# Performance work log

Measured on AMD Instinct MI355X. Metric: run time of the kernel, lower is better.

The kernel has to match this reference:

```python
import jax, jax.numpy as jnp
import numpy as np

N_NODES = 50000
N_EDGES = 500000
F_IN = 16      # node feature dim F
F_OUT = 16     # channels F_
E_FEAT = 8     # edge feature dim
HIDDEN = 32    # kernel_network hidden size


def _glorot(key, shape):
    fan_in, fan_out = shape[0], shape[1]
    lim = np.sqrt(6.0 / (fan_in + fan_out)).astype(np.float32)
    return jax.random.uniform(key, shape, jnp.float32, -lim, lim)


def setup_inputs() -> dict:
    key = jax.random.key(0)
    ks = jax.random.split(key, 8)
    x = jax.random.normal(ks[0], (N_NODES, F_IN), jnp.float32)
    e = jax.random.uniform(ks[1], (N_EDGES, E_FEAT), jnp.float32)
    idx_i = jax.random.randint(ks[2], (N_EDGES,), 0, N_NODES, jnp.int32)  # targets
    idx_j = jax.random.randint(ks[3], (N_EDGES,), 0, N_NODES, jnp.int32)  # sources
    W1 = _glorot(ks[4], (E_FEAT, HIDDEN))
    b1 = jnp.zeros((HIDDEN,), jnp.float32)
    W2 = _glorot(ks[5], (HIDDEN, F_OUT * F_IN))
    b2 = jnp.zeros((F_OUT * F_IN,), jnp.float32)
    root_kernel = _glorot(ks[6], (F_IN, F_OUT))
    bias = jnp.zeros((F_OUT,), jnp.float32)
    return {"x": x, "e": e, "idx_i": idx_i, "idx_j": idx_j,
            "W1": W1, "b1": b1, "W2": W2, "b2": b2,
            "root_kernel": root_kernel, "bias": bias}


def reference(x, e, idx_i, idx_j, W1, b1, W2, b2, root_kernel, bias):
    # Edge-conditioned filter-generating network (MLP, relu hidden, linear out)
    h = jax.nn.relu(e @ W1 + b1)                       # [E, HIDDEN]
    kern = (h @ W2 + b2).reshape(-1, F_IN, F_OUT)      # [E, F, F_]
    # gather source node features, per-edge matmul, scatter-add to targets
    msg = jnp.einsum('ef,efc->ec', x[idx_j], kern)     # [E, F_]
    out = jax.ops.segment_sum(msg, idx_i, num_segments=N_NODES)  # [N, F_]
    out = out + x @ root_kernel + bias
    return out
```

## Files before the change

kernel.cpp:

```cpp
#include <hip/hip_runtime.h>

typedef __attribute__((ext_vector_type(8))) _Float16 f16x8_t;
typedef __attribute__((ext_vector_type(2))) _Float16 f16x2_t;
typedef __attribute__((ext_vector_type(4))) float f32x4_t;

__device__ __forceinline__ f16x2_t pkh(float lo, float hi) {
    return __builtin_bit_cast(f16x2_t, __builtin_amdgcn_cvt_pkrtz(lo, hi));
}
__device__ __forceinline__ unsigned int pkrtz(float lo, float hi) {
    return __builtin_bit_cast(unsigned int, __builtin_amdgcn_cvt_pkrtz(lo, hi));
}

#define LD4(p) (*reinterpret_cast<const float4*>(p))


__global__ __launch_bounds__(256) void prep_kernel(
    const float* __restrict__ x,
    const float* __restrict__ W1,
    const float* __restrict__ b1,
    const float* __restrict__ W2,
    const float* __restrict__ b2,
    const float* __restrict__ rootk,
    const float* __restrict__ bias,
    float* __restrict__ out,
    _Float16* __restrict__ tab,
    int n_nodes, int root_blocks)
{
    const int tid = threadIdx.x;
    const int bid = blockIdx.x;

    if (bid < root_blocks) {
        __shared__ float sR[256];
        __shared__ float sB[16];
        if (tid < 256) sR[tid] = rootk[tid];
        if (tid < 16)  sB[tid] = bias[tid];
        __syncthreads();

        int nid = bid * 256 + tid;
        if (nid >= n_nodes) return;

        const float* xp = x + (size_t)nid * 16;
        float xf[16];
#pragma unroll
        for (int f = 0; f < 16; f += 4) {
            float4 v = LD4(xp + f);
            xf[f] = v.x; xf[f + 1] = v.y; xf[f + 2] = v.z; xf[f + 3] = v.w;
        }
        float o[16];
#pragma unroll
        for (int cc = 0; cc < 16; ++cc) o[cc] = sB[cc];
#pragma unroll
        for (int f = 0; f < 16; ++f) {
            float p = xf[f];
#pragma unroll
            for (int cc = 0; cc < 16; ++cc)
                o[cc] = fmaf(p, sR[f * 16 + cc], o[cc]);
        }
        float* dst = out + (size_t)nid * 16;
#pragma unroll
        for (int cc = 0; cc < 16; cc += 4)
            *reinterpret_cast<float4*>(dst + cc) = make_float4(o[cc], o[cc+1], o[cc+2], o[cc+3]);
    } else {
        for (int it = tid; it < 64 * 19; it += 256) {
            int grp  = it >> 6;
            int lane = it & 63;
            int q = lane >> 4, cc = lane & 15;
            union { _Float16 h[8]; uint4 u; } pk;
            if (grp < 2) {
                int hh = grp;
#pragma unroll
                for (int j = 0; j < 8; ++j) {
                    float v = 0.f;
                    if (q == 0)              v = W1[j * 32 + cc + 16 * hh];
                    else if (q == 1 && j==0) v = b1[cc + 16 * hh];
                    pk.h[j] = (_Float16)v;
                }
                *reinterpret_cast<uint4*>(tab + ((size_t)hh * 64 + lane) * 8) = pk.u;
            } else {
                int s = grp - 2;
#pragma unroll
                for (int j = 0; j < 8; ++j) {
                    float v;
                    if (s < 16) {
                        int hd = (j < 4) ? (4 * q + j) : (4 * q + 12 + j);
                        v = W2[hd * 256 + s * 16 + cc];
                    } else {
                        v = (q < 2) ? b2[(q * 8 + j) * 16 + cc] : 0.f;
                    }
                    pk.h[j] = (_Float16)v;
                }
                *reinterpret_cast<uint4*>(tab + 1024 + ((size_t)s * 64 + lane) * 8) = pk.u;
            }
        }
    }
}

__device__ __forceinline__ float4 shfl4(float4 v, int src) {
    float4 r;
    r.x = __shfl(v.x, src); r.y = __shfl(v.y, src);
    r.z = __shfl(v.z, src); r.w = __shfl(v.w, src);
    return r;
}

template<int EXACT>
__global__ __launch_bounds__(256) void edge_mfma_kernel(
    const float* __restrict__ x,
    const float* __restrict__ efeat,
    const int*   __restrict__ idx_i,
    const int*   __restrict__ idx_j,
    const _Float16* __restrict__ tab,
    float* __restrict__ out,
    int n_edges, int n_groups)
{
    const int lane = threadIdx.x & 63;
    const int q = lane >> 4;
    const int c = lane & 15;

    const f16x8_t* w1f = reinterpret_cast<const f16x8_t*>(tab) + lane;
    const f16x8_t aW1_0 = w1f[0];
    const f16x8_t aW1_1 = w1f[64];
    const f16x8_t* w2f = reinterpret_cast<const f16x8_t*>(tab + 1024) + lane;
    f16x8_t bW2[17];
#pragma unroll
    for (int s = 0; s < 17; ++s) bW2[s] = w2f[s * 64];

    const unsigned int c1 = (q == 1) ? 0x00003C00u : 0u;
    const bool isq0 = (q == 0);
    const bool qodd = (q & 1);
    float* const outc = out + c;

    const int wid = blockIdx.x * 4 + (threadIdx.x >> 6);
    const int g0  = wid * 4;
    if (g0 >= n_groups) return;
    const int rem = n_groups - g0;

    auto ldj = [&](int gg) -> int {
        int eid = gg * 16 + c;
        if (!EXACT) { if (eid >= n_edges) eid = n_edges - 1; }
        return idx_j[eid];
    };
    auto eptr = [&](int gg) -> const float* {
        int eid = gg * 16 + c;
        if (!EXACT) { if (eid >= n_edges) eid = n_edges - 1; }
        return efeat + (size_t)eid * 8;
    };

    auto compute = [&](float4 XQ, float4 E0, float4 E1, int gg) {
        int t0, t1, t2, t3;
        if (EXACT || (gg * 16 + 16 <= n_edges)) {
            int4 tv = *reinterpret_cast<const int4*>(idx_i + gg * 16 + q * 4);
            t0 = tv.x; t1 = tv.y; t2 = tv.z; t3 = tv.w;
        } else {
            const int eb = gg * 16 + q * 4;
            t0 = (eb + 0 < n_edges) ? idx_i[eb + 0] : 0;
            t1 = (eb + 1 < n_edges) ? idx_i[eb + 1] : 0;
            t2 = (eb + 2 < n_edges) ? idx_i[eb + 2] : 0;
            t3 = (eb + 3 < n_edges) ? idx_i[eb + 3] : 0;
        }

        float4 X0 = shfl4(XQ, c);
        float4 X1 = shfl4(XQ, c + 16);
        float4 X2 = shfl4(XQ, c + 32);
        float4 X3 = shfl4(XQ, c + 48);

        union { f16x8_t v8; f16x2_t v2[4]; unsigned int u[4]; } bB;
        bB.u[0] = isq0 ? pkrtz(E0.x, E0.y) : c1;
        bB.u[1] = isq0 ? pkrtz(E0.z, E0.w) : 0u;
        bB.u[2] = isq0 ? pkrtz(E1.x, E1.y) : 0u;
        bB.u[3] = isq0 ? pkrtz(E1.z, E1.w) : 0u;

        f32x4_t z4 = {0.f, 0.f, 0.f, 0.f};
        f32x4_t h0 = __builtin_amdgcn_mfma_f32_16x16x32_f16(aW1_0, bB.v8, z4, 0, 0, 0);
        f32x4_t h1 = __builtin_amdgcn_mfma_f32_16x16x32_f16(aW1_1, bB.v8, z4, 0, 0, 0);

        f16x2_t hp0 = pkh(fmaxf(h0[0], 0.f), fmaxf(h0[1], 0.f));
        f16x2_t hp1 = pkh(fmaxf(h0[2], 0.f), fmaxf(h0[3], 0.f));
        f16x2_t hp2 = pkh(fmaxf(h1[0], 0.f), fmaxf(h1[1], 0.f));
        f16x2_t hp3 = pkh(fmaxf(h1[2], 0.f), fmaxf(h1[3], 0.f));

        float xf[16];
        xf[0]=X0.x; xf[1]=X0.y; xf[2]=X0.z; xf[3]=X0.w;
        xf[4]=X1.x; xf[5]=X1.y; xf[6]=X1.z; xf[7]=X1.w;
        xf[8]=X2.x; xf[9]=X2.y; xf[10]=X2.z; xf[11]=X2.w;
        xf[12]=X3.x; xf[13]=X3.y; xf[14]=X3.z; xf[15]=X3.w;

        f16x2_t xss[16];
#pragma unroll
        for (int f = 0; f < 16; ++f)
            xss[f] = pkh(xf[f], xf[f]);

        union { f16x8_t v8; unsigned int u[4]; } xb;
        xb.u[0] = pkrtz(qodd ? xf[8]  : xf[0], qodd ? xf[9]  : xf[1]);
        xb.u[1] = pkrtz(qodd ? xf[10] : xf[2], qodd ? xf[11] : xf[3]);
        xb.u[2] = pkrtz(qodd ? xf[12] : xf[4], qodd ? xf[13] : xf[5]);
        xb.u[3] = pkrtz(qodd ? xf[14] : xf[6], qodd ? xf[15] : xf[7]);

        f32x4_t acc0 = {0.f, 0.f, 0.f, 0.f};
        f32x4_t acc1 = {0.f, 0.f, 0.f, 0.f};
        union { f16x8_t v8; f16x2_t v2[4]; } afr;
#pragma unroll
        for (int s = 0; s < 16; s += 2) {
            f16x2_t xs2 = xss[s];
            afr.v2[0] = hp0 * xs2;
            afr.v2[1] = hp1 * xs2;
            afr.v2[2] = hp2 * xs2;
            afr.v2[3] = hp3 * xs2;
            acc0 = __builtin_amdgcn_mfma_f32_16x16x32_f16(afr.v8, bW2[s], acc0, 0, 0, 0);
            xs2 = xss[s + 1];
            afr.v2[0] = hp0 * xs2;
            afr.v2[1] = hp1 * xs2;
            afr.v2[2] = hp2 * xs2;
            afr.v2[3] = hp3 * xs2;
            acc1 = __builtin_amdgcn_mfma_f32_16x16x32_f16(afr.v8, bW2[s + 1], acc1, 0, 0, 0);
        }
        acc0 = __builtin_amdgcn_mfma_f32_16x16x32_f16(xb.v8, bW2[16], acc0, 0, 0, 0);

        const float rr0 = acc0[0] + acc1[0];
        const float rr1 = acc0[1] + acc1[1];
        const float rr2 = acc0[2] + acc1[2];
        const float rr3 = acc0[3] + acc1[3];
        if (EXACT) {
            atomicAdd(outc + (size_t)t0 * 16, rr0);
            atomicAdd(outc + (size_t)t1 * 16, rr1);
            atomicAdd(outc + (size_t)t2 * 16, rr2);
            atomicAdd(outc + (size_t)t3 * 16, rr3);
        } else {
            const int eb = gg * 16 + q * 4;
            if (eb + 0 < n_edges) atomicAdd(outc + (size_t)t0 * 16, rr0);
            if (eb + 1 < n_edges) atomicAdd(outc + (size_t)t1 * 16, rr1);
            if (eb + 2 < n_edges) atomicAdd(outc + (size_t)t2 * 16, rr2);
            if (eb + 3 < n_edges) atomicAdd(outc + (size_t)t3 * 16, rr3);
        }
    };

#define STAGE(BXQ, BE0, BE1, jv, gg)                                \
    {                                                               \
        BXQ = LD4(x + (size_t)(jv) * 16 + q * 4);                   \
        const float* ep = eptr(gg);                                 \
        BE0 = LD4(ep); BE1 = LD4(ep + 4);                           \
    }

    const int jA = ldj(g0);
    const int jB = (rem > 1) ? ldj(g0 + 1) : 0;
    const int jC = (rem > 2) ? ldj(g0 + 2) : 0;
    const int jD = (rem > 3) ? ldj(g0 + 3) : 0;

    float4 aq, ae0, ae1;
    float4 bq, be0, be1;

    STAGE(aq, ae0, ae1, jA, g0);
    if (rem > 1) STAGE(bq, be0, be1, jB, g0 + 1);
    compute(aq, ae0, ae1, g0);
    if (rem > 1) {
        if (rem > 2) STAGE(aq, ae0, ae1, jC, g0 + 2);
        compute(bq, be0, be1, g0 + 1);
        if (rem > 2) {
            if (rem > 3) STAGE(bq, be0, be1, jD, g0 + 3);
            compute(aq, ae0, ae1, g0 + 2);
            if (rem > 3) compute(bq, be0, be1, g0 + 3);
        }
    }
#undef STAGE
}

extern "C" void kernel_launch(void* const* d_in, const int* in_sizes, int n_in,
                              void* d_out, int out_size, void* d_ws, size_t ws_size,
                              hipStream_t stream) {
    const float* x     = (const float*)d_in[0];
    const float* e     = (const float*)d_in[1];
    const int*   idx_i = (const int*)d_in[2];
    const int*   idx_j = (const int*)d_in[3];
    const float* W1    = (const float*)d_in[4];
    const float* b1    = (const float*)d_in[5];
    const float* W2    = (const float*)d_in[6];
    const float* b2    = (const float*)d_in[7];
    const float* rootk = (const float*)d_in[8];
    const float* bias  = (const float*)d_in[9];

    int n_nodes  = in_sizes[0] / 16;
    int n_edges  = in_sizes[2];
    int n_groups = (n_edges + 15) / 16;

    float* out = (float*)d_out;
    _Float16* tab = (_Float16*)d_ws;

    int root_blocks = (n_nodes + 255) / 256;
    prep_kernel<<<root_blocks + 1, 256, 0, stream>>>(x, W1, b1, W2, b2, rootk, bias,
                                                     out, tab, n_nodes, root_blocks);

    int blocks = (n_groups + 15) / 16;
    if ((n_edges & 15) == 0)
        edge_mfma_kernel<1><<<blocks, 256, 0, stream>>>(x, e, idx_i, idx_j, tab, out,
                                                        n_edges, n_groups);
    else
        edge_mfma_kernel<0><<<blocks, 256, 0, stream>>>(x, e, idx_i, idx_j, tab, out,
                                                        n_edges, n_groups);
}
```

Measured before the change: 46.22 us.

## Bucket edges by target node to reduce scatter atomics

Adds a bucketing pass that atomically counts each edge's target and stores edge ids in fixed per-node slots, with an overflow list handled by a scalar fallback kernel. A node-centric MFMA kernel then processes each node's incoming edges, reduces the messages in registers, and issues one atomic per output channel per node instead of one per edge. The old edge kernel is kept as a fallback when the workspace is too small and is changed to a grid-stride form. The cost is an extra pass with 500k atomics, a scattered write of edge ids, and poor wave utilisation: average degree is about 10, so each wave runs one 16-edge chunk per node with many lanes idle, and edge features are now gathered randomly.

```diff
diff --git a/kernel.cpp b/kernel.cpp
--- a/kernel.cpp
+++ b/kernel.cpp
@@ -4,6 +4,9 @@
 typedef __attribute__((ext_vector_type(2))) _Float16 f16x2_t;
 typedef __attribute__((ext_vector_type(4))) float f32x4_t;
 
+#define SLOTS 64
+#define OVF_CAP 8192
+
 __device__ __forceinline__ f16x2_t pkh(float lo, float hi) {
     return __builtin_bit_cast(f16x2_t, __builtin_amdgcn_cvt_pkrtz(lo, hi));
 }
@@ -12,6 +15,13 @@
 }
 
 #define LD4(p) (*reinterpret_cast<const float4*>(p))
+
+__device__ __forceinline__ float4 shfl4(float4 v, int src) {
+    float4 r;
+    r.x = __shfl(v.x, src); r.y = __shfl(v.y, src);
+    r.z = __shfl(v.z, src); r.w = __shfl(v.w, src);
+    return r;
+}
 
 
 __global__ __launch_bounds__(256) void prep_kernel(
@@ -24,6 +34,8 @@
     const float* __restrict__ bias,
     float* __restrict__ out,
     _Float16* __restrict__ tab,
+    int* __restrict__ cnt,
+    int* __restrict__ ovf_cnt,
     int n_nodes, int root_blocks)
 {
     const int tid = threadIdx.x;
@@ -38,6 +50,7 @@
 
         int nid = bid * 256 + tid;
         if (nid >= n_nodes) return;
+        if (cnt) cnt[nid] = 0;
 
         const float* xp = x + (size_t)nid * 16;
         float xf[16];
@@ -61,6 +74,7 @@
         for (int cc = 0; cc < 16; cc += 4)
             *reinterpret_cast<float4*>(dst + cc) = make_float4(o[cc], o[cc+1], o[cc+2], o[cc+3]);
     } else {
+        if (tid == 0 && ovf_cnt) *ovf_cnt = 0;
         for (int it = tid; it < 64 * 19; it += 256) {
             int grp  = it >> 6;
             int lane = it & 63;
@@ -95,27 +109,190 @@
     }
 }
 
-__device__ __forceinline__ float4 shfl4(float4 v, int src) {
-    float4 r;
-    r.x = __shfl(v.x, src); r.y = __shfl(v.y, src);
-    r.z = __shfl(v.z, src); r.w = __shfl(v.w, src);
-    return r;
-}
-
-template<int EXACT>
-__global__ __launch_bounds__(256) void edge_mfma_kernel(
+__global__ __launch_bounds__(256) void bucket_kernel(
+    const int* __restrict__ idx_i,
+    int* __restrict__ cnt,
+    int* __restrict__ eord,
+    int* __restrict__ ovf_cnt,
+    int* __restrict__ ovf,
+    int n_edges)
+{
+    int e = blockIdx.x * 256 + threadIdx.x;
+    if (e >= n_edges) return;
+    int t = idx_i[e];
+    int pos = atomicAdd(cnt + t, 1);
+    if (pos < SLOTS) {
+        eord[(size_t)t * SLOTS + pos] = e;
+    } else {
+        int o = atomicAdd(ovf_cnt, 1);
+        if (o < OVF_CAP) ovf[o] = e;
+    }
+}
+
+__global__ __launch_bounds__(256) void node_mfma_kernel(
+    const float* __restrict__ x,
+    const float* __restrict__ efeat,
+    const int*   __restrict__ idx_j,
+    const _Float16* __restrict__ tab,
+    const int*   __restrict__ cnt,
+    const int*   __restrict__ eord,
+    float* __restrict__ out,
+    int n_nodes)
+{
+    const int lane = threadIdx.x & 63;
+    const int q = lane >> 4;
+    const int c = lane & 15;
+
+    const f16x8_t* w1f = reinterpret_cast<const f16x8_t*>(tab) + lane;
+    const f16x8_t aW1_0 = w1f[0];
+    const f16x8_t aW1_1 = w1f[64];
+    const f16x8_t* w2f = reinterpret_cast<const f16x8_t*>(tab + 1024) + lane;
+    f16x8_t bW2[17];
+#pragma unroll
+    for (int s = 0; s < 17; ++s) bW2[s] = w2f[s * 64];
+
+    const unsigned int c1 = (q == 1) ? 0x00003C00u : 0u;
+    const bool isq0 = (q == 0);
+    const bool qodd = (q & 1);
+
+    const int wid = blockIdx.x * 4 + (threadIdx.x >> 6);
+    const int n0 = wid * 4;
+    if (n0 >= n_nodes) return;
+
+    for (int nn = 0; nn < 4; ++nn) {
+        const int n = n0 + nn;
+        if (n >= n_nodes) break;
+        const int deg = cnt[n];
+        if (deg <= 0) continue;
+        const int degc = (deg < SLOTS) ? deg : SLOTS;
+
+        const int* ebase = eord + (size_t)n * SLOTS;
+
+        f32x4_t acc0 = {0.f, 0.f, 0.f, 0.f};
+        f32x4_t acc1 = {0.f, 0.f, 0.f, 0.f};
+
+        for (int k0 = 0; k0 < degc; k0 += 16) {
+            const int k = k0 + c;
+            const bool valid = (k < degc);
+            const int eid = valid ? ebase[k] : ebase[0];
+            const int j = idx_j[eid];
+
+            float4 XQ = LD4(x + (size_t)j * 16 + q * 4);
+            float4 X0 = shfl4(XQ, c);
+            float4 X1 = shfl4(XQ, c + 16);
+            float4 X2 = shfl4(XQ, c + 32);
+            float4 X3 = shfl4(XQ, c + 48);
+
+            const float* ep = efeat + (size_t)eid * 8;
+            float4 E0 = LD4(ep), E1 = LD4(ep + 4);
+
+            union { f16x8_t v8; unsigned int u[4]; } bB;
+            bB.u[0] = isq0 ? pkrtz(E0.x, E0.y) : c1;
+            bB.u[1] = isq0 ? pkrtz(E0.z, E0.w) : 0u;
+            bB.u[2] = isq0 ? pkrtz(E1.x, E1.y) : 0u;
+            bB.u[3] = isq0 ? pkrtz(E1.z, E1.w) : 0u;
+
+            f32x4_t z4 = {0.f, 0.f, 0.f, 0.f};
+            f32x4_t h0 = __builtin_amdgcn_mfma_f32_16x16x32_f16(aW1_0, bB.v8, z4, 0, 0, 0);
+            f32x4_t h1 = __builtin_amdgcn_mfma_f32_16x16x32_f16(aW1_1, bB.v8, z4, 0, 0, 0);
+
+            f16x2_t hp0 = pkh(fmaxf(h0[0], 0.f), fmaxf(h0[1], 0.f));
+            f16x2_t hp1 = pkh(fmaxf(h0[2], 0.f), fmaxf(h0[3], 0.f));
+            f16x2_t hp2 = pkh(fmaxf(h1[0], 0.f), fmaxf(h1[1], 0.f));
+            f16x2_t hp3 = pkh(fmaxf(h1[2], 0.f), fmaxf(h1[3], 0.f));
+
+            float xf[16];
+            xf[0]=X0.x; xf[1]=X0.y; xf[2]=X0.z; xf[3]=X0.w;
+            xf[4]=X1.x; xf[5]=X1.y; xf[6]=X1.z; xf[7]=X1.w;
+            xf[8]=X2.x; xf[9]=X2.y; xf[10]=X2.z; xf[11]=X2.w;
+            xf[12]=X3.x; xf[13]=X3.y; xf[14]=X3.z; xf[15]=X3.w;
+            if (!valid) {
+#pragma unroll
+                for (int t = 0; t < 16; ++t) xf[t] = 0.f;
+            }
+
+            f16x2_t xss[16];
+#pragma unroll
+            for (int f = 0; f < 16; ++f)
+                xss[f] = pkh(xf[f], xf[f]);
+
+            union { f16x8_t v8; unsigned int u[4]; } xb;
+            xb.u[0] = pkrtz(qodd ? xf[8]  : xf[0], qodd ? xf[9]  : xf[1]);
+            xb.u[1] = pkrtz(qodd ? xf[10] : xf[2], qodd ? xf[11] : xf[3]);
+            xb.u[2] = pkrtz(qodd ? xf[12] : xf[4], qodd ? xf[13] : xf[5]);
+            xb.u[3] = pkrtz(qodd ? xf[14] : xf[6], qodd ? xf[15] : xf[7]);
+
+            union { f16x8_t v8; f16x2_t v2[4]; } afr;
+#pragma unroll
+            for (int s = 0; s < 16; s += 2) {
+                f16x2_t xs2 = xss[s];
+                afr.v2[0] = hp0 * xs2;
+                afr.v2[1] = hp1 * xs2;
+                afr.v2[2] = hp2 * xs2;
+                afr.v2[3] = hp3 * xs2;
+                acc0 = __builtin_amdgcn_mfma_f32_16x16x32_f16(afr.v8, bW2[s], acc0, 0, 0, 0);
+                xs2 = xss[s + 1];
+                afr.v2[0] = hp0 * xs2;
+                afr.v2[1] = hp1 * xs2;
+                afr.v2[2] = hp2 * xs2;
+                afr.v2[3] = hp3 * xs2;
+                acc1 = __builtin_amdgcn_mfma_f32_16x16x32_f16(afr.v8, bW2[s + 1], acc1, 0, 0, 0);
+            }
+            acc0 = __builtin_amdgcn_mfma_f32_16x16x32_f16(xb.v8, bW2[16], acc0, 0, 0, 0);
+        }
+
+        float s = (acc0[0] + acc1[0]) + (acc0[1] + acc1[1])
+                + (acc0[2] + acc1[2]) + (acc0[3] + acc1[3]);
+        s += __shfl_xor(s, 16);
+        s += __shfl_xor(s, 32);
+        if (lane < 16)
+            atomicAdd(out + (size_t)n * 16 + c, s);
+    }
+}
+
+__global__ __launch_bounds__(256) void ovf_kernel(
     const float* __restrict__ x,
     const float* __restrict__ efeat,
     const int*   __restrict__ idx_i,
     const int*   __restrict__ idx_j,
-    const _Float16* __restrict__ tab,
-    float* __restrict__ out,
+    const float* __restrict__ W1, const float* __restrict__ b1,
+    const float* __restrict__ W2, const float* __restrict__ b2,
+    const int*   __restrict__ ovf_cnt,
+    const int*   __restrict__ ovf,
+    float* __restrict__ out)
+{
+    int m = *ovf_cnt;
+    if (m > OVF_CAP) m = OVF_CAP;
+    if (m <= 0) return;
+    for (int it = threadIdx.x; it < m * 16; it += 256) {
+        int o = it >> 4, cch = it & 15;
+        int e = ovf[o];
+        int j = idx_j[e];
+        int t = idx_i[e];
+        float msg = 0.f;
+        for (int hd = 0; hd < 32; ++hd) {
+            float h = b1[hd];
+            for (int k = 0; k < 8; ++k) h = fmaf(efeat[(size_t)e*8+k], W1[k*32+hd], h);
+            h = fmaxf(h, 0.f);
+            float dot = 0.f;
+            for (int f = 0; f < 16; ++f) dot = fmaf(x[(size_t)j*16+f], W2[hd*256 + f*16 + cch], dot);
+            msg = fmaf(h, dot, msg);
+        }
+        for (int f = 0; f < 16; ++f) msg = fmaf(x[(size_t)j*16+f], b2[f*16+cch], msg);
+        atomicAdd(out + (size_t)t * 16 + cch, msg);
+    }
+}
+
+template<int EXACT>
+__global__ __launch_bounds__(256) void edge_mfma_kernel(
+    const float* __restrict__ x, const float* __restrict__ efeat,
+    const int* __restrict__ idx_i, const int* __restrict__ idx_j,
+    const _Float16* __restrict__ tab, float* __restrict__ out,
     int n_edges, int n_groups)
 {
     const int lane = threadIdx.x & 63;
     const int q = lane >> 4;
     const int c = lane & 15;
-
     const f16x8_t* w1f = reinterpret_cast<const f16x8_t*>(tab) + lane;
     const f16x8_t aW1_0 = w1f[0];
     const f16x8_t aW1_1 = w1f[64];
@@ -123,144 +300,78 @@
     f16x8_t bW2[17];
 #pragma unroll
     for (int s = 0; s < 17; ++s) bW2[s] = w2f[s * 64];
-
     const unsigned int c1 = (q == 1) ? 0x00003C00u : 0u;
     const bool isq0 = (q == 0);
     const bool qodd = (q & 1);
     float* const outc = out + c;
 
-    const int wid = blockIdx.x * 4 + (threadIdx.x >> 6);
-    const int g0  = wid * 4;
-    if (g0 >= n_groups) return;
-    const int rem = n_groups - g0;
-
-    auto ldj = [&](int gg) -> int {
-        int eid = gg * 16 + c;
-        if (!EXACT) { if (eid >= n_edges) eid = n_edges - 1; }
-        return idx_j[eid];
-    };
-    auto eptr = [&](int gg) -> const float* {
-        int eid = gg * 16 + c;
-        if (!EXACT) { if (eid >= n_edges) eid = n_edges - 1; }
-        return efeat + (size_t)eid * 8;
-    };
-
-    auto compute = [&](float4 XQ, float4 E0, float4 E1, int gg) {
+    for (int g = blockIdx.x * 4 + (threadIdx.x >> 6); g < n_groups; g += gridDim.x * 4) {
+        int eid = g * 16 + c;
+        bool va = (eid < n_edges);
+        int el = va ? eid : (n_edges - 1);
+        int j = idx_j[el];
+        float4 X0 = LD4(x + (size_t)j*16), X1 = LD4(x + (size_t)j*16 + 4);
+        float4 X2 = LD4(x + (size_t)j*16 + 8), X3 = LD4(x + (size_t)j*16 + 12);
+        const float* ep = efeat + (size_t)el * 8;
+        float4 E0 = LD4(ep), E1 = LD4(ep + 4);
         int t0, t1, t2, t3;
-        if (EXACT || (gg * 16 + 16 <= n_edges)) {
-            int4 tv = *reinterpret_cast<const int4*>(idx_i + gg * 16 + q * 4);
-            t0 = tv.x; t1 = tv.y; t2 = tv.z; t3 = tv.w;
-        } else {
-            const int eb = gg * 16 + q * 4;
+        {
+            const int eb = g * 16 + q * 4;
             t0 = (eb + 0 < n_edges) ? idx_i[eb + 0] : 0;
             t1 = (eb + 1 < n_edges) ? idx_i[eb + 1] : 0;
             t2 = (eb + 2 < n_edges) ? idx_i[eb + 2] : 0;
             t3 = (eb + 3 < n_edges) ? idx_i[eb + 3] : 0;
         }
-
-        float4 X0 = shfl4(XQ, c);
-        float4 X1 = shfl4(XQ, c + 16);
-        float4 X2 = shfl4(XQ, c + 32);
-        float4 X3 = shfl4(XQ, c + 48);
-
-        union { f16x8_t v8; f16x2_t v2[4]; unsigned int u[4]; } bB;
+        union { f16x8_t v8; unsigned int u[4]; } bB;
         bB.u[0] = isq0 ? pkrtz(E0.x, E0.y) : c1;
         bB.u[1] = isq0 ? pkrtz(E0.z, E0.w) : 0u;
         bB.u[2] = isq0 ? pkrtz(E1.x, E1.y) : 0u;
         bB.u[3] = isq0 ? pkrtz(E1.z, E1.w) : 0u;
-
         f32x4_t z4 = {0.f, 0.f, 0.f, 0.f};
         f32x4_t h0 = __builtin_amdgcn_mfma_f32_16x16x32_f16(aW1_0, bB.v8, z4, 0, 0, 0);
         f32x4_t h1 = __builtin_amdgcn_mfma_f32_16x16x32_f16(aW1_1, bB.v8, z4, 0, 0, 0);
-
         f16x2_t hp0 = pkh(fmaxf(h0[0], 0.f), fmaxf(h0[1], 0.f));
         f16x2_t hp1 = pkh(fmaxf(h0[2], 0.f), fmaxf(h0[3], 0.f));
         f16x2_t hp2 = pkh(fmaxf(h1[0], 0.f), fmaxf(h1[1], 0.f));
         f16x2_t hp3 = pkh(fmaxf(h1[2], 0.f), fmaxf(h1[3], 0.f));
-
         float xf[16];
         xf[0]=X0.x; xf[1]=X0.y; xf[2]=X0.z; xf[3]=X0.w;
         xf[4]=X1.x; xf[5]=X1.y; xf[6]=X1.z; xf[7]=X1.w;
         xf[8]=X2.x; xf[9]=X2.y; xf[10]=X2.z; xf[11]=X2.w;
         xf[12]=X3.x; xf[13]=X3.y; xf[14]=X3.z; xf[15]=X3.w;
-
+        if (!va) { for (int t = 0; t < 16; ++t) xf[t] = 0.f; }
         f16x2_t xss[16];
 #pragma unroll
-        for (int f = 0; f < 16; ++f)
-            xss[f] = pkh(xf[f], xf[f]);
-
+        for (int f = 0; f < 16; ++f) xss[f] = pkh(xf[f], xf[f]);
         union { f16x8_t v8; unsigned int u[4]; } xb;
         xb.u[0] = pkrtz(qodd ? xf[8]  : xf[0], qodd ? xf[9]  : xf[1]);
         xb.u[1] = pkrtz(qodd ? xf[10] : xf[2], qodd ? xf[11] : xf[3]);
         xb.u[2] = pkrtz(qodd ? xf[12] : xf[4], qodd ? xf[13] : xf[5]);
         xb.u[3] = pkrtz(qodd ? xf[14] : xf[6], qodd ? xf[15] : xf[7]);
-
-        f32x4_t acc0 = {0.f, 0.f, 0.f, 0.f};
-        f32x4_t acc1 = {0.f, 0.f, 0.f, 0.f};
+        f32x4_t acc0 = {0.f,0.f,0.f,0.f}, acc1 = {0.f,0.f,0.f,0.f};
         union { f16x8_t v8; f16x2_t v2[4]; } afr;
 #pragma unroll
         for (int s = 0; s < 16; s += 2) {
             f16x2_t xs2 = xss[s];
-            afr.v2[0] = hp0 * xs2;
-            afr.v2[1] = hp1 * xs2;
-            afr.v2[2] = hp2 * xs2;
-            afr.v2[3] = hp3 * xs2;
+            afr.v2[0] = hp0 * xs2; afr.v2[1] = hp1 * xs2;
+            afr.v2[2] = hp2 * xs2; afr.v2[3] = hp3 * xs2;
             acc0 = __builtin_amdgcn_mfma_f32_16x16x32_f16(afr.v8, bW2[s], acc0, 0, 0, 0);
             xs2 = xss[s + 1];
-            afr.v2[0] = hp0 * xs2;
-            afr.v2[1] = hp1 * xs2;
-            afr.v2[2] = hp2 * xs2;
-            afr.v2[3] = hp3 * xs2;
+            afr.v2[0] = hp0 * xs2; afr.v2[1] = hp1 * xs2;
+            afr.v2[2] = hp2 * xs2; afr.v2[3] = hp3 * xs2;
             acc1 = __builtin_amdgcn_mfma_f32_16x16x32_f16(afr.v8, bW2[s + 1], acc1, 0, 0, 0);
         }
         acc0 = __builtin_amdgcn_mfma_f32_16x16x32_f16(xb.v8, bW2[16], acc0, 0, 0, 0);
-
         const float rr0 = acc0[0] + acc1[0];
         const float rr1 = acc0[1] + acc1[1];
         const float rr2 = acc0[2] + acc1[2];
         const float rr3 = acc0[3] + acc1[3];
-        if (EXACT) {
-            atomicAdd(outc + (size_t)t0 * 16, rr0);
-            atomicAdd(outc + (size_t)t1 * 16, rr1);
-            atomicAdd(outc + (size_t)t2 * 16, rr2);
-            atomicAdd(outc + (size_t)t3 * 16, rr3);
-        } else {
-            const int eb = gg * 16 + q * 4;
-            if (eb + 0 < n_edges) atomicAdd(outc + (size_t)t0 * 16, rr0);
-            if (eb + 1 < n_edges) atomicAdd(outc + (size_t)t1 * 16, rr1);
-            if (eb + 2 < n_edges) atomicAdd(outc + (size_t)t2 * 16, rr2);
-            if (eb + 3 < n_edges) atomicAdd(outc + (size_t)t3 * 16, rr3);
-        }
-    };
-
-#define STAGE(BXQ, BE0, BE1, jv, gg)                                \
-    {                                                               \
-        BXQ = LD4(x + (size_t)(jv) * 16 + q * 4);                   \
-        const float* ep = eptr(gg);                                 \
-        BE0 = LD4(ep); BE1 = LD4(ep + 4);                           \
-    }
-
-    const int jA = ldj(g0);
-    const int jB = (rem > 1) ? ldj(g0 + 1) : 0;
-    const int jC = (rem > 2) ? ldj(g0 + 2) : 0;
-    const int jD = (rem > 3) ? ldj(g0 + 3) : 0;
-
-    float4 aq, ae0, ae1;
-    float4 bq, be0, be1;
-
-    STAGE(aq, ae0, ae1, jA, g0);
-    if (rem > 1) STAGE(bq, be0, be1, jB, g0 + 1);
-    compute(aq, ae0, ae1, g0);
-    if (rem > 1) {
-        if (rem > 2) STAGE(aq, ae0, ae1, jC, g0 + 2);
-        compute(bq, be0, be1, g0 + 1);
-        if (rem > 2) {
-            if (rem > 3) STAGE(bq, be0, be1, jD, g0 + 3);
-            compute(aq, ae0, ae1, g0 + 2);
-            if (rem > 3) compute(bq, be0, be1, g0 + 3);
-        }
-    }
-#undef STAGE
+        const int eb = g * 16 + q * 4;
+        if (eb + 0 < n_edges) atomicAdd(outc + (size_t)t0 * 16, rr0);
+        if (eb + 1 < n_edges) atomicAdd(outc + (size_t)t1 * 16, rr1);
+        if (eb + 2 < n_edges) atomicAdd(outc + (size_t)t2 * 16, rr2);
+        if (eb + 3 < n_edges) atomicAdd(outc + (size_t)t3 * 16, rr3);
+    }
 }
 
 extern "C" void kernel_launch(void* const* d_in, const int* in_sizes, int n_in,
@@ -279,20 +390,39 @@
 
     int n_nodes  = in_sizes[0] / 16;
     int n_edges  = in_sizes[2];
-    int n_groups = (n_edges + 15) / 16;
 
     float* out = (float*)d_out;
     _Float16* tab = (_Float16*)d_ws;
+    int* cnt     = (int*)((char*)d_ws + 65536);
+    int* ovf_cnt = (int*)((char*)d_ws + 266240);
+    int* ovf     = (int*)((char*)d_ws + 266304);
+    int* eord    = (int*)((char*)d_ws + 524288);
+
+    size_t need = 524288 + (size_t)n_nodes * SLOTS * sizeof(int);
+    const int use_bucket = (ws_size >= need) ? 1 : 0;
 
     int root_blocks = (n_nodes + 255) / 256;
     prep_kernel<<<root_blocks + 1, 256, 0, stream>>>(x, W1, b1, W2, b2, rootk, bias,
-                                                     out, tab, n_nodes, root_blocks);
-
-    int blocks = (n_groups + 15) / 16;
-    if ((n_edges & 15) == 0)
-        edge_mfma_kernel<1><<<blocks, 256, 0, stream>>>(x, e, idx_i, idx_j, tab, out,
-                                                        n_edges, n_groups);
-    else
-        edge_mfma_kernel<0><<<blocks, 256, 0, stream>>>(x, e, idx_i, idx_j, tab, out,
-                                                        n_edges, n_groups);
-}
+                                                     out, tab, use_bucket ? cnt : nullptr,
+                                                     use_bucket ? ovf_cnt : nullptr,
+                                                     n_nodes, root_blocks);
+
+    if (use_bucket) {
+        int bblocks = (n_edges + 255) / 256;
+        bucket_kernel<<<bblocks, 256, 0, stream>>>(idx_i, cnt, eord, ovf_cnt, ovf, n_edges);
+        int nblocks = (n_nodes + 15) / 16;
+        node_mfma_kernel<<<nblocks, 256, 0, stream>>>(x, e, idx_j, tab, cnt, eord,
+                                                      out, n_nodes);
+        ovf_kernel<<<1, 256, 0, stream>>>(x, e, idx_i, idx_j, W1, b1, W2, b2,
+                                          ovf_cnt, ovf, out);
+    } else {
+        int n_groups = (n_edges + 15) / 16;
+        int blocks = (n_groups + 63) / 64;
+        if ((n_edges & 15) == 0)
+            edge_mfma_kernel<1><<<blocks * 16, 256, 0, stream>>>(x, e, idx_i, idx_j, tab,
+                                                                 out, n_edges, n_groups);
+        else
+            edge_mfma_kernel<0><<<blocks * 16, 256, 0, stream>>>(x, e, idx_i, idx_j, tab,
+                                                                 out, n_edges, n_groups);
+    }
+}
```

Measured after the change: 97.38 us. 111% more time.

## Pre-gather source features and edge features into fp16 buffers in a separate pass

Applied to the files above, without the earlier changes.

Adds a pre-pass kernel that gathers x[idx_j] per edge and converts it and the edge features to packed fp16 in workspace buffers. The main MFMA kernel then reads these contiguous records instead of doing a random gather plus cross-lane shuffles, and it runs as a grid-stride loop over 1024 blocks. This removes the shuffle and conversion work from the compute kernel. In exchange it adds an extra launch and a full round trip of roughly 48 bytes per edge through memory, and drops the explicit two-stage load pipelining. A fallback kernel is kept for when the workspace is too small.

```diff
diff --git a/kernel.cpp b/kernel.cpp
--- a/kernel.cpp
+++ b/kernel.cpp
@@ -9,6 +9,12 @@
 }
 __device__ __forceinline__ unsigned int pkrtz(float lo, float hi) {
     return __builtin_bit_cast(unsigned int, __builtin_amdgcn_cvt_pkrtz(lo, hi));
+}
+__device__ __forceinline__ f16x2_t dup_lo(unsigned int u) {
+    return __builtin_bit_cast(f16x2_t, __builtin_amdgcn_perm(u, u, 0x01000100u));
+}
+__device__ __forceinline__ f16x2_t dup_hi(unsigned int u) {
+    return __builtin_bit_cast(f16x2_t, __builtin_amdgcn_perm(u, u, 0x03020302u));
 }
 
 #define LD4(p) (*reinterpret_cast<const float4*>(p))
@@ -95,19 +101,42 @@
     }
 }
 
-__device__ __forceinline__ float4 shfl4(float4 v, int src) {
-    float4 r;
-    r.x = __shfl(v.x, src); r.y = __shfl(v.y, src);
-    r.z = __shfl(v.z, src); r.w = __shfl(v.w, src);
-    return r;
-}
-
-template<int EXACT>
-__global__ __launch_bounds__(256) void edge_mfma_kernel(
+__global__ __launch_bounds__(256) void prepg_kernel(
     const float* __restrict__ x,
     const float* __restrict__ efeat,
-    const int*   __restrict__ idx_i,
     const int*   __restrict__ idx_j,
+    unsigned int* __restrict__ rec32,
+    unsigned int* __restrict__ ef16,
+    int n_edges)
+{
+    int e = blockIdx.x * 256 + threadIdx.x;
+    if (e >= n_edges) return;
+
+    const int j = idx_j[e];
+    const float* xp = x + (size_t)j * 16;
+    float4 x0 = LD4(xp), x1 = LD4(xp + 4), x2 = LD4(xp + 8), x3 = LD4(xp + 12);
+
+    uint4 r0, r1;
+    r0.x = pkrtz(x0.x, x0.y); r0.y = pkrtz(x0.z, x0.w);
+    r0.z = pkrtz(x1.x, x1.y); r0.w = pkrtz(x1.z, x1.w);
+    r1.x = pkrtz(x2.x, x2.y); r1.y = pkrtz(x2.z, x2.w);
+    r1.z = pkrtz(x3.x, x3.y); r1.w = pkrtz(x3.z, x3.w);
+    uint4* rp = reinterpret_cast<uint4*>(rec32 + (size_t)e * 8);
+    rp[0] = r0; rp[1] = r1;
+
+    const float* ep = efeat + (size_t)e * 8;
+    float4 e0 = LD4(ep), e1 = LD4(ep + 4);
+    uint4 re;
+    re.x = pkrtz(e0.x, e0.y); re.y = pkrtz(e0.z, e0.w);
+    re.z = pkrtz(e1.x, e1.y); re.w = pkrtz(e1.z, e1.w);
+    *reinterpret_cast<uint4*>(ef16 + (size_t)e * 4) = re;
+}
+
+template<int EXACT>
+__global__ __launch_bounds__(256) void edge_pre_kernel(
+    const unsigned int* __restrict__ rec32,
+    const unsigned int* __restrict__ ef16,
+    const int* __restrict__ idx_i,
     const _Float16* __restrict__ tab,
     float* __restrict__ out,
     int n_edges, int n_groups)
@@ -129,45 +158,43 @@
     const bool qodd = (q & 1);
     float* const outc = out + c;
 
-    const int wid = blockIdx.x * 4 + (threadIdx.x >> 6);
-    const int g0  = wid * 4;
-    if (g0 >= n_groups) return;
-    const int rem = n_groups - g0;
-
-    auto ldj = [&](int gg) -> int {
-        int eid = gg * 16 + c;
+    const int nwaves = gridDim.x * 4;
+    for (int g = blockIdx.x * 4 + (threadIdx.x >> 6); g < n_groups; g += nwaves) {
+        int eid = g * 16 + c;
         if (!EXACT) { if (eid >= n_edges) eid = n_edges - 1; }
-        return idx_j[eid];
-    };
-    auto eptr = [&](int gg) -> const float* {
-        int eid = gg * 16 + c;
-        if (!EXACT) { if (eid >= n_edges) eid = n_edges - 1; }
-        return efeat + (size_t)eid * 8;
-    };
-
-    auto compute = [&](float4 XQ, float4 E0, float4 E1, int gg) {
+
+        const uint4* rp = reinterpret_cast<const uint4*>(rec32 + (size_t)eid * 8);
+        uint4 r0 = rp[0], r1 = rp[1];
+        uint4 re = *reinterpret_cast<const uint4*>(ef16 + (size_t)eid * 4);
+
         int t0, t1, t2, t3;
-        if (EXACT || (gg * 16 + 16 <= n_edges)) {
-            int4 tv = *reinterpret_cast<const int4*>(idx_i + gg * 16 + q * 4);
+        {
+            int4 tv;
+            if (EXACT || (g * 16 + 16 <= n_edges)) {
+                tv = *reinterpret_cast<const int4*>(idx_i + g * 16 + q * 4);
+            } else {
+                const int eb = g * 16 + q * 4;
+                tv.x = (eb + 0 < n_edges) ? idx_i[eb + 0] : 0;
+                tv.y = (eb + 1 < n_edges) ? idx_i[eb + 1] : 0;
+                tv.z = (eb + 2 < n_edges) ? idx_i[eb + 2] : 0;
+                tv.w = (eb + 3 < n_edges) ? idx_i[eb + 3] : 0;
+            }
             t0 = tv.x; t1 = tv.y; t2 = tv.z; t3 = tv.w;
-        } else {
-            const int eb = gg * 16 + q * 4;
-            t0 = (eb + 0 < n_edges) ? idx_i[eb + 0] : 0;
-            t1 = (eb + 1 < n_edges) ? idx_i[eb + 1] : 0;
-            t2 = (eb + 2 < n_edges) ? idx_i[eb + 2] : 0;
-            t3 = (eb + 3 < n_edges) ? idx_i[eb + 3] : 0;
-        }
-
-        float4 X0 = shfl4(XQ, c);
-        float4 X1 = shfl4(XQ, c + 16);
-        float4 X2 = shfl4(XQ, c + 32);
-        float4 X3 = shfl4(XQ, c + 48);
-
-        union { f16x8_t v8; f16x2_t v2[4]; unsigned int u[4]; } bB;
-        bB.u[0] = isq0 ? pkrtz(E0.x, E0.y) : c1;
-        bB.u[1] = isq0 ? pkrtz(E0.z, E0.w) : 0u;
-        bB.u[2] = isq0 ? pkrtz(E1.x, E1.y) : 0u;
-        bB.u[3] = isq0 ? pkrtz(E1.z, E1.w) : 0u;
+        }
+
+        unsigned int pr[8] = {r0.x, r0.y, r0.z, r0.w, r1.x, r1.y, r1.z, r1.w};
+        if (!EXACT) {
+            if (g * 16 + c >= n_edges) {
+#pragma unroll
+                for (int t = 0; t < 8; ++t) pr[t] = 0u;
+            }
+        }
+
+        union { f16x8_t v8; unsigned int u[4]; } bB;
+        bB.u[0] = isq0 ? re.x : c1;
+        bB.u[1] = isq0 ? re.y : 0u;
+        bB.u[2] = isq0 ? re.z : 0u;
+        bB.u[3] = isq0 ? re.w : 0u;
 
         f32x4_t z4 = {0.f, 0.f, 0.f, 0.f};
         f32x4_t h0 = __builtin_amdgcn_mfma_f32_16x16x32_f16(aW1_0, bB.v8, z4, 0, 0, 0);
@@ -178,40 +205,30 @@
         f16x2_t hp2 = pkh(fmaxf(h1[0], 0.f), fmaxf(h1[1], 0.f));
         f16x2_t hp3 = pkh(fmaxf(h1[2], 0.f), fmaxf(h1[3], 0.f));
 
-        float xf[16];
-        xf[0]=X0.x; xf[1]=X0.y; xf[2]=X0.z; xf[3]=X0.w;
-        xf[4]=X1.x; xf[5]=X1.y; xf[6]=X1.z; xf[7]=X1.w;
-        xf[8]=X2.x; xf[9]=X2.y; xf[10]=X2.z; xf[11]=X2.w;
-        xf[12]=X3.x; xf[13]=X3.y; xf[14]=X3.z; xf[15]=X3.w;
-
-        f16x2_t xss[16];
-#pragma unroll
-        for (int f = 0; f < 16; ++f)
-            xss[f] = pkh(xf[f], xf[f]);
-
         union { f16x8_t v8; unsigned int u[4]; } xb;
-        xb.u[0] = pkrtz(qodd ? xf[8]  : xf[0], qodd ? xf[9]  : xf[1]);
-        xb.u[1] = pkrtz(qodd ? xf[10] : xf[2], qodd ? xf[11] : xf[3]);
-        xb.u[2] = pkrtz(qodd ? xf[12] : xf[4], qodd ? xf[13] : xf[5]);
-        xb.u[3] = pkrtz(qodd ? xf[14] : xf[6], qodd ? xf[15] : xf[7]);
+        xb.u[0] = qodd ? pr[4] : pr[0];
+        xb.u[1] = qodd ? pr[5] : pr[1];
+        xb.u[2] = qodd ? pr[6] : pr[2];
+        xb.u[3] = qodd ? pr[7] : pr[3];
 
         f32x4_t acc0 = {0.f, 0.f, 0.f, 0.f};
         f32x4_t acc1 = {0.f, 0.f, 0.f, 0.f};
         union { f16x8_t v8; f16x2_t v2[4]; } afr;
 #pragma unroll
-        for (int s = 0; s < 16; s += 2) {
-            f16x2_t xs2 = xss[s];
-            afr.v2[0] = hp0 * xs2;
-            afr.v2[1] = hp1 * xs2;
-            afr.v2[2] = hp2 * xs2;
-            afr.v2[3] = hp3 * xs2;
-            acc0 = __builtin_amdgcn_mfma_f32_16x16x32_f16(afr.v8, bW2[s], acc0, 0, 0, 0);
-            xs2 = xss[s + 1];
-            afr.v2[0] = hp0 * xs2;
-            afr.v2[1] = hp1 * xs2;
-            afr.v2[2] = hp2 * xs2;
-            afr.v2[3] = hp3 * xs2;
-            acc1 = __builtin_amdgcn_mfma_f32_16x16x32_f16(afr.v8, bW2[s + 1], acc1, 0, 0, 0);
+        for (int s2 = 0; s2 < 8; ++s2) {
+            const unsigned int pp = pr[s2];
+            f16x2_t xlo = dup_lo(pp);
+            afr.v2[0] = hp0 * xlo;
+            afr.v2[1] = hp1 * xlo;
+            afr.v2[2] = hp2 * xlo;
+            afr.v2[3] = hp3 * xlo;
+            acc0 = __builtin_amdgcn_mfma_f32_16x16x32_f16(afr.v8, bW2[2 * s2], acc0, 0, 0, 0);
+            f16x2_t xhi = dup_hi(pp);
+            afr.v2[0] = hp0 * xhi;
+            afr.v2[1] = hp1 * xhi;
+            afr.v2[2] = hp2 * xhi;
+            afr.v2[3] = hp3 * xhi;
+            acc1 = __builtin_amdgcn_mfma_f32_16x16x32_f16(afr.v8, bW2[2 * s2 + 1], acc1, 0, 0, 0);
         }
         acc0 = __builtin_amdgcn_mfma_f32_16x16x32_f16(xb.v8, bW2[16], acc0, 0, 0, 0);
 
@@ -225,42 +242,103 @@
             atomicAdd(outc + (size_t)t2 * 16, rr2);
             atomicAdd(outc + (size_t)t3 * 16, rr3);
         } else {
-            const int eb = gg * 16 + q * 4;
+            const int eb = g * 16 + q * 4;
             if (eb + 0 < n_edges) atomicAdd(outc + (size_t)t0 * 16, rr0);
             if (eb + 1 < n_edges) atomicAdd(outc + (size_t)t1 * 16, rr1);
             if (eb + 2 < n_edges) atomicAdd(outc + (size_t)t2 * 16, rr2);
             if (eb + 3 < n_edges) atomicAdd(outc + (size_t)t3 * 16, rr3);
         }
-    };
-
-#define STAGE(BXQ, BE0, BE1, jv, gg)                                \
-    {                                                               \
-        BXQ = LD4(x + (size_t)(jv) * 16 + q * 4);                   \
-        const float* ep = eptr(gg);                                 \
-        BE0 = LD4(ep); BE1 = LD4(ep + 4);                           \
     }
-
-    const int jA = ldj(g0);
-    const int jB = (rem > 1) ? ldj(g0 + 1) : 0;
-    const int jC = (rem > 2) ? ldj(g0 + 2) : 0;
-    const int jD = (rem > 3) ? ldj(g0 + 3) : 0;
-
-    float4 aq, ae0, ae1;
-    float4 bq, be0, be1;
-
-    STAGE(aq, ae0, ae1, jA, g0);
-    if (rem > 1) STAGE(bq, be0, be1, jB, g0 + 1);
-    compute(aq, ae0, ae1, g0);
-    if (rem > 1) {
-        if (rem > 2) STAGE(aq, ae0, ae1, jC, g0 + 2);
-        compute(bq, be0, be1, g0 + 1);
-        if (rem > 2) {
-            if (rem > 3) STAGE(bq, be0, be1, jD, g0 + 3);
-            compute(aq, ae0, ae1, g0 + 2);
-            if (rem > 3) compute(bq, be0, be1, g0 + 3);
-        }
+}
+
+__global__ __launch_bounds__(256) void edge_fallback_kernel(
+    const float* __restrict__ x, const float* __restrict__ efeat,
+    const int* __restrict__ idx_i, const int* __restrict__ idx_j,
+    const _Float16* __restrict__ tab, float* __restrict__ out,
+    int n_edges, int n_groups)
+{
+    const int lane = threadIdx.x & 63;
+    const int q = lane >> 4;
+    const int c = lane & 15;
+    const f16x8_t* w1f = reinterpret_cast<const f16x8_t*>(tab) + lane;
+    const f16x8_t aW1_0 = w1f[0];
+    const f16x8_t aW1_1 = w1f[64];
+    const f16x8_t* w2f = reinterpret_cast<const f16x8_t*>(tab + 1024) + lane;
+    f16x8_t bW2[17];
+#pragma unroll
+    for (int s = 0; s < 17; ++s) bW2[s] = w2f[s * 64];
+    const unsigned int c1 = (q == 1) ? 0x00003C00u : 0u;
+    const bool isq0 = (q == 0);
+    const bool qodd = (q & 1);
+    float* const outc = out + c;
+
+    for (int g = blockIdx.x * 4 + (threadIdx.x >> 6); g < n_groups; g += gridDim.x * 4) {
+        int eid = g * 16 + c;
+        bool va = (eid < n_edges);
+        int el = va ? eid : (n_edges - 1);
+        int j = idx_j[el];
+        float4 X0 = LD4(x + (size_t)j*16), X1 = LD4(x + (size_t)j*16 + 4);
+        float4 X2 = LD4(x + (size_t)j*16 + 8), X3 = LD4(x + (size_t)j*16 + 12);
+        const float* ep = efeat + (size_t)el * 8;
+        float4 E0 = LD4(ep), E1 = LD4(ep + 4);
+        int t0, t1, t2, t3;
+        {
+            const int eb = g * 16 + q * 4;
+            t0 = (eb + 0 < n_edges) ? idx_i[eb + 0] : 0;
+            t1 = (eb + 1 < n_edges) ? idx_i[eb + 1] : 0;
+            t2 = (eb + 2 < n_edges) ? idx_i[eb + 2] : 0;
+            t3 = (eb + 3 < n_edges) ? idx_i[eb + 3] : 0;
+        }
+        union { f16x8_t v8; unsigned int u[4]; } bB;
+        bB.u[0] = isq0 ? pkrtz(E0.x, E0.y) : c1;
+        bB.u[1] = isq0 ? pkrtz(E0.z, E0.w) : 0u;
+        bB.u[2] = isq0 ? pkrtz(E1.x, E1.y) : 0u;
+        bB.u[3] = isq0 ? pkrtz(E1.z, E1.w) : 0u;
+        f32x4_t z4 = {0.f, 0.f, 0.f, 0.f};
+        f32x4_t h0 = __builtin_amdgcn_mfma_f32_16x16x32_f16(aW1_0, bB.v8, z4, 0, 0, 0);
+        f32x4_t h1 = __builtin_amdgcn_mfma_f32_16x16x32_f16(aW1_1, bB.v8, z4, 0, 0, 0);
+        f16x2_t hp0 = pkh(fmaxf(h0[0], 0.f), fmaxf(h0[1], 0.f));
+        f16x2_t hp1 = pkh(fmaxf(h0[2], 0.f), fmaxf(h0[3], 0.f));
+        f16x2_t hp2 = pkh(fmaxf(h1[0], 0.f), fmaxf(h1[1], 0.f));
+        f16x2_t hp3 = pkh(fmaxf(h1[2], 0.f), fmaxf(h1[3], 0.f));
+        float xf[16];
+        xf[0]=X0.x; xf[1]=X0.y; xf[2]=X0.z; xf[3]=X0.w;
+        xf[4]=X1.x; xf[5]=X1.y; xf[6]=X1.z; xf[7]=X1.w;
+        xf[8]=X2.x; xf[9]=X2.y; xf[10]=X2.z; xf[11]=X2.w;
+        xf[12]=X3.x; xf[13]=X3.y; xf[14]=X3.z; xf[15]=X3.w;
+        if (!va) { for (int t = 0; t < 16; ++t) xf[t] = 0.f; }
+        f16x2_t xss[16];
+#pragma unroll
+        for (int f = 0; f < 16; ++f) xss[f] = pkh(xf[f], xf[f]);
+        union { f16x8_t v8; unsigned int u[4]; } xb;
+        xb.u[0] = pkrtz(qodd ? xf[8]  : xf[0], qodd ? xf[9]  : xf[1]);
+        xb.u[1] = pkrtz(qodd ? xf[10] : xf[2], qodd ? xf[11] : xf[3]);
+        xb.u[2] = pkrtz(qodd ? xf[12] : xf[4], qodd ? xf[13] : xf[5]);
+        xb.u[3] = pkrtz(qodd ? xf[14] : xf[6], qodd ? xf[15] : xf[7]);
+        f32x4_t acc0 = {0.f,0.f,0.f,0.f}, acc1 = {0.f,0.f,0.f,0.f};
+        union { f16x8_t v8; f16x2_t v2[4]; } afr;
+#pragma unroll
+        for (int s = 0; s < 16; s += 2) {
+            f16x2_t xs2 = xss[s];
+            afr.v2[0] = hp0 * xs2; afr.v2[1] = hp1 * xs2;
+            afr.v2[2] = hp2 * xs2; afr.v2[3] = hp3 * xs2;
+            acc0 = __builtin_amdgcn_mfma_f32_16x16x32_f16(afr.v8, bW2[s], acc0, 0, 0, 0);
+            xs2 = xss[s + 1];
+            afr.v2[0] = hp0 * xs2; afr.v2[1] = hp1 * xs2;
+            afr.v2[2] = hp2 * xs2; afr.v2[3] = hp3 * xs2;
+            acc1 = __builtin_amdgcn_mfma_f32_16x16x32_f16(afr.v8, bW2[s + 1], acc1, 0, 0, 0);
+        }
+        acc0 = __builtin_amdgcn_mfma_f32_16x16x32_f16(xb.v8, bW2[16], acc0, 0, 0, 0);
+        const float rr0 = acc0[0] + acc1[0];
+        const float rr1 = acc0[1] + acc1[1];
+        const float rr2 = acc0[2] + acc1[2];
+        const float rr3 = acc0[3] + acc1[3];
+        const int eb = g * 16 + q * 4;
+        if (eb + 0 < n_edges) atomicAdd(outc + (size_t)t0 * 16, rr0);
+        if (eb + 1 < n_edges) atomicAdd(outc + (size_t)t1 * 16, rr1);
+        if (eb + 2 < n_edges) atomicAdd(outc + (size_t)t2 * 16, rr2);
+        if (eb + 3 < n_edges) atomicAdd(outc + (size_t)t3 * 16, rr3);
     }
-#undef STAGE
 }
 
 extern "C" void kernel_launch(void* const* d_in, const int* in_sizes, int n_in,
@@ -283,16 +361,27 @@
 
     float* out = (float*)d_out;
     _Float16* tab = (_Float16*)d_ws;
+    unsigned int* rec32 = (unsigned int*)((char*)d_ws + (1u << 20));
+    unsigned int* ef16  = (unsigned int*)((char*)d_ws + (20u << 20));
+
+    size_t need = (20u << 20) + (size_t)n_edges * 16;
+    const int use_pre = (ws_size >= need) ? 1 : 0;
 
     int root_blocks = (n_nodes + 255) / 256;
     prep_kernel<<<root_blocks + 1, 256, 0, stream>>>(x, W1, b1, W2, b2, rootk, bias,
                                                      out, tab, n_nodes, root_blocks);
 
-    int blocks = (n_groups + 15) / 16;
-    if ((n_edges & 15) == 0)
-        edge_mfma_kernel<1><<<blocks, 256, 0, stream>>>(x, e, idx_i, idx_j, tab, out,
-                                                        n_edges, n_groups);
-    else
-        edge_mfma_kernel<0><<<blocks, 256, 0, stream>>>(x, e, idx_i, idx_j, tab, out,
-                                                        n_edges, n_groups);
-}
+    if (use_pre) {
+        int gblocks = (n_edges + 255) / 256;
+        prepg_kernel<<<gblocks, 256, 0, stream>>>(x, e, idx_j, rec32, ef16, n_edges);
+        if ((n_edges & 15) == 0)
+            edge_pre_kernel<1><<<1024, 256, 0, stream>>>(rec32, ef16, idx_i, tab, out,
+                                                         n_edges, n_groups);
+        else
+            edge_pre_kernel<0><<<1024, 256, 0, stream>>>(rec32, ef16, idx_i, tab, out,
+                                                         n_edges, n_groups);
+    } else {
+        edge_fallback_kernel<<<1024, 256, 0, stream>>>(x, e, idx_i, idx_j, tab, out,
+                                                       n_edges, n_groups);
+    }
+}
```

Result: slower. 56.16 us (+21.5%).
